# Optimization experiments

Measured on AMD Instinct MI355X. Metric: run time of the kernel, lower is better.

The kernel has to match this reference:

```python
import jax, jax.numpy as jnp
import numpy as np

N_NODES = 100000
N_EDGES = 800000
IN_DIM = 128
HID_DIM = 128


def setup_inputs() -> dict:
    key = jax.random.key(0)
    ks = jax.random.split(key, 10)
    s = 0.05
    return {
        "x": jax.random.normal(ks[0], (N_NODES, IN_DIM), dtype=jnp.float32),
        "edge_index": jax.random.randint(ks[1], (2, N_EDGES), 0, N_NODES, dtype=jnp.int64),
        "W1l": jax.random.normal(ks[2], (HID_DIM, IN_DIM), dtype=jnp.float32) * s,
        "b1": jax.random.normal(ks[3], (HID_DIM,), dtype=jnp.float32) * s,
        "W1r": jax.random.normal(ks[4], (HID_DIM, IN_DIM), dtype=jnp.float32) * s,
        "W2l": jax.random.normal(ks[5], (HID_DIM, HID_DIM), dtype=jnp.float32) * s,
        "b2": jax.random.normal(ks[6], (HID_DIM,), dtype=jnp.float32) * s,
        "W2r": jax.random.normal(ks[7], (HID_DIM, HID_DIM), dtype=jnp.float32) * s,
        "Wfc": jax.random.normal(ks[8], (1, HID_DIM), dtype=jnp.float32) * s,
        "bfc": jax.random.normal(ks[9], (1,), dtype=jnp.float32) * s,
    }


def _sage_conv(h, src, dst, n_nodes, Wl, b, Wr):
    # PyG SAGEConv (mean aggr): lin_l(mean_{j in N(i)} x_j) + lin_r(x_i)
    msg = h[src]  # [E, D] gather from source nodes
    agg = jax.ops.segment_sum(msg, dst, num_segments=n_nodes)  # [N, D]
    cnt = jax.ops.segment_sum(jnp.ones((src.shape[0], 1), h.dtype), dst,
                              num_segments=n_nodes)  # [N, 1]
    mean = agg / jnp.maximum(cnt, 1.0)  # isolated nodes -> 0 (matches scatter-mean)
    return mean @ Wl.T + b + h @ Wr.T


def reference(x, edge_index, W1l, b1, W1r, W2l, b2, W2r, Wfc, bfc):
    src, dst = edge_index[0], edge_index[1]
    n = x.shape[0]
    h = jax.nn.relu(_sage_conv(x, src, dst, n, W1l, b1, W1r))
    h = jax.nn.relu(_sage_conv(h, src, dst, n, W2l, b2, W2r))
    # dropout is identity in eval mode
    out = h @ Wfc.T + bfc  # [N, 1]
    return out.squeeze(-1)  # [N]
```

## Files before the change

### kernel.cpp

```cpp
#include <hip/hip_runtime.h>

#define N_NODES 100000
#define N_EDGES 800000
#define DIM 128

#define NB 391
#define BKCAP 2560
#define EPB 2048
#define BINB ((N_EDGES + EPB - 1) / EPB)
#define NXD (N_NODES * DIM / 2)

typedef __attribute__((ext_vector_type(8))) short short8;
typedef __attribute__((ext_vector_type(4))) float float4v;
typedef __attribute__((ext_vector_type(2))) float float2v;
typedef __attribute__((ext_vector_type(4))) unsigned int uint4v;

__device__ __forceinline__ float lo16(unsigned int v) {
    return __uint_as_float(v << 16);
}
__device__ __forceinline__ float hi16(unsigned int v) {
    return __uint_as_float(v & 0xffff0000u);
}
__device__ __forceinline__ float2v unp(unsigned int v) {
    return (float2v){lo16(v), hi16(v)};
}
__device__ __forceinline__ unsigned short f2bf(float f) {
    unsigned int x = __float_as_uint(f);
    unsigned int r = x + 0x7fffu + ((x >> 16) & 1u);
    return (unsigned short)(r >> 16);
}
__device__ __forceinline__ unsigned int packbf(float a, float b) {
    return (unsigned int)f2bf(a) | ((unsigned int)f2bf(b) << 16);
}

__device__ __forceinline__ int wave_iscan(int x, int lane) {
#pragma unroll
    for (int off = 1; off < 64; off <<= 1) {
        int n = __shfl_up(x, off, 64);
        x += (lane >= off) ? n : 0;
    }
    return x;
}


__global__ void edet_kernel(const int* __restrict__ edge, int* __restrict__ flags,
                            int* __restrict__ cur) {
    int i = blockIdx.x * blockDim.x + threadIdx.x;
    if (i < NB) cur[i] = 0;
    if (edge[2 * i + 1] != 0) flags[1] = 1;
}


__device__ __forceinline__ void load_edge(const int* __restrict__ edge, int eflag, int e,
                                          int& s, int& d) {
    if (eflag == 0) {
        s = edge[2 * e];
        d = edge[2 * (N_EDGES + e)];
    } else {
        s = edge[e];
        d = edge[N_EDGES + e];
    }
}


__global__ __launch_bounds__(256) void binconv_kernel(
    const int* __restrict__ edge, const int* __restrict__ flags, int* __restrict__ cur,
    unsigned int* __restrict__ pairs, const float* __restrict__ x,
    const float* __restrict__ wa, const float* __restrict__ wb,
    const float* __restrict__ wc, const float* __restrict__ wd,
    unsigned int* __restrict__ xdst, unsigned int* __restrict__ wdst) {
    int t = threadIdx.x;
    if (blockIdx.x >= BINB) {
        int i = (blockIdx.x - BINB) * 256 + t;
        if (i < NXD) {
            float2 v = ((const float2*)x)[i];
            xdst[i] = packbf(v.x, v.y);
        } else {
            int j = i - NXD;
            if (j < 4 * 8192) {
                int m = j >> 13, r = j & 8191;
                const float* src = (m == 0) ? wa : (m == 1) ? wb : (m == 2) ? wc : wd;
                float2 v = ((const float2*)src)[r];
                wdst[j] = packbf(v.x, v.y);
            }
        }
        return;
    }
    __shared__ int lcnt[NB];
    __shared__ int lbase[NB];
    for (int i = t; i < NB; i += 256) lcnt[i] = 0;
    __syncthreads();
    int e0 = blockIdx.x * EPB;
    int eflag = (flags[1] == 1) ? 1 : 0;
    int vb[8];
    unsigned int vp[8];
    bool valid[8];
#pragma unroll
    for (int k = 0; k < 8; ++k) {
        int e = e0 + k * 256 + t;
        valid[k] = false;
        if (e < N_EDGES) {
            int s, d;
            load_edge(edge, eflag, e, s, d);
            if ((unsigned)s < N_NODES && (unsigned)d < N_NODES) {
                valid[k] = true;
                vb[k] = d >> 8;
                vp[k] = ((unsigned int)s << 8) | (unsigned int)(d & 255);
                atomicAdd(&lcnt[vb[k]], 1);
            }
        }
    }
    __syncthreads();
    for (int i = t; i < NB; i += 256) {
        int c = lcnt[i];
        lbase[i] = (c > 0) ? atomicAdd(&cur[i], c) : 0;
        lcnt[i] = 0;
    }
    __syncthreads();
#pragma unroll
    for (int k = 0; k < 8; ++k) {
        if (valid[k]) {
            int b = vb[k];
            int pos = lbase[b] + atomicAdd(&lcnt[b], 1);
            if (pos < BKCAP)
                pairs[(size_t)b * BKCAP + pos] = vp[k];
        }
    }
}


__global__ __launch_bounds__(256) void csr_kernel(const int* __restrict__ cur,
                                                  const unsigned int* __restrict__ pairs,
                                                  int* __restrict__ rowptr,
                                                  int* __restrict__ esrc) {
    __shared__ int sh[512];
    __shared__ int hist[256];
    __shared__ int wsum[8];
    int b = blockIdx.x, t = threadIdx.x;
    int lane = t & 63, wv = t >> 6;
    int e0 = 2 * t, e1 = 2 * t + 1;
    int v0 = (e0 < NB) ? min(cur[e0], BKCAP) : 0;
    int v1 = (e1 < NB) ? min(cur[e1], BKCAP) : 0;
    int p = wave_iscan(v0 + v1, lane);
    if (lane == 63) wsum[wv] = p;
    hist[t] = 0;
    __syncthreads();
    int wpre = 0;
#pragma unroll
    for (int w = 0; w < 4; ++w) wpre += (w < wv) ? wsum[w] : 0;
    int incl1 = wpre + p;
    sh[e0] = incl1 - v1;
    sh[e1] = incl1;
    __syncthreads();
    int n = min(cur[b], BKCAP);
    int base = sh[b] - n;
    if (b == 0 && t == 0) rowptr[N_NODES] = sh[NB - 1];
    const unsigned int* pp = pairs + (size_t)b * BKCAP;
    for (int i = t; i < n; i += 256) atomicAdd(&hist[pp[i] & 255u], 1);
    __syncthreads();
    int v = hist[t];
    int ix = wave_iscan(v, lane);
    if (lane == 63) wsum[4 + wv] = ix;
    __syncthreads();
    int wpre2 = 0;
#pragma unroll
    for (int w = 0; w < 4; ++w) wpre2 += (w < wv) ? wsum[4 + w] : 0;
    int excl = wpre2 + ix - v;
    int node = b * 256 + t;
    if (node < N_NODES) rowptr[node] = base + excl;
    hist[t] = excl;
    __syncthreads();
    for (int i = t; i < n; i += 256) {
        unsigned int pk = pp[i];
        int pos = atomicAdd(&hist[pk & 255u], 1);
        esrc[base + pos] = (int)(pk >> 8);
    }
}


__global__ __launch_bounds__(256) void agg_kernel(const unsigned int* __restrict__ feat2,
                                                  const int* __restrict__ rowptr,
                                                  const int* __restrict__ esrc,
                                                  unsigned int* __restrict__ meanout) {
    int wid = (blockIdx.x * blockDim.x + threadIdx.x) >> 6;
    int lane = threadIdx.x & 63;
    int rowgrp = lane >> 4;
    int dimgrp = lane & 15;
    const int nwaves = 2048 * 4;
    for (int node = wid; node < N_NODES; node += nwaves) {
        int beg = rowptr[node], end = rowptr[node + 1];
        float2v a0 = {0.f, 0.f}, a1 = {0.f, 0.f}, a2 = {0.f, 0.f}, a3 = {0.f, 0.f};
        int e = beg;
        for (; e + 8 <= end; e += 8) {
            int s0 = esrc[e + rowgrp];
            int s1 = esrc[e + 4 + rowgrp];
            uint4v v0 = *(const uint4v*)(feat2 + (size_t)s0 * 64 + dimgrp * 4);
            uint4v v1 = *(const uint4v*)(feat2 + (size_t)s1 * 64 + dimgrp * 4);
            a0 += unp(v0.x) + unp(v1.x);
            a1 += unp(v0.y) + unp(v1.y);
            a2 += unp(v0.z) + unp(v1.z);
            a3 += unp(v0.w) + unp(v1.w);
        }
        if (e < end) {
            int i0 = e + rowgrp, i1 = e + 4 + rowgrp;
            bool ok0 = i0 < end, ok1 = i1 < end;
            int s0 = esrc[ok0 ? i0 : end - 1];
            int s1 = esrc[ok1 ? i1 : end - 1];
            uint4v v0 = *(const uint4v*)(feat2 + (size_t)s0 * 64 + dimgrp * 4);
            uint4v v1 = *(const uint4v*)(feat2 + (size_t)s1 * 64 + dimgrp * 4);
            float m0 = ok0 ? 1.f : 0.f, m1 = ok1 ? 1.f : 0.f;
            float2v m0v = {m0, m0}, m1v = {m1, m1};
            a0 += m0v * unp(v0.x) + m1v * unp(v1.x);
            a1 += m0v * unp(v0.y) + m1v * unp(v1.y);
            a2 += m0v * unp(v0.z) + m1v * unp(v1.z);
            a3 += m0v * unp(v0.w) + m1v * unp(v1.w);
        }
        float2v s0v = (rowgrp & 1) ? a0 : a1;
        float2v k0v = (rowgrp & 1) ? a1 : a0;
        float2v s2v = (rowgrp & 1) ? a2 : a3;
        float2v k2v = (rowgrp & 1) ? a3 : a2;
        k0v.x += __shfl_xor(s0v.x, 16, 64);
        k0v.y += __shfl_xor(s0v.y, 16, 64);
        k2v.x += __shfl_xor(s2v.x, 16, 64);
        k2v.y += __shfl_xor(s2v.y, 16, 64);
        float2v sv = (rowgrp & 2) ? k0v : k2v;
        float2v kv = (rowgrp & 2) ? k2v : k0v;
        kv.x += __shfl_xor(sv.x, 32, 64);
        kv.y += __shfl_xor(sv.y, 32, 64);
        int deg = end - beg;
        float sc = deg > 0 ? 1.f / (float)deg : 0.f;
        meanout[(size_t)node * 64 + dimgrp * 4 + rowgrp] = packbf(kv.x * sc, kv.y * sc);
    }
}


template <int FUSE_FC>
__global__ __launch_bounds__(256, 2) void gemm_kernel(
    const unsigned short* __restrict__ A0, const unsigned short* __restrict__ A1,
    const unsigned int* __restrict__ Wpk,
    const float* __restrict__ bias, const float* __restrict__ wfc,
    const float* __restrict__ bfc, unsigned short* __restrict__ hout,
    float* __restrict__ out) {
    __shared__ unsigned int wlds[16384];

    {
        int mat = threadIdx.x >> 7, row = threadIdx.x & 127;
        const unsigned int* g = Wpk + mat * 8192 + row * 64;
        unsigned int* lbase = wlds + mat * 8192;
#pragma unroll
        for (int q = 0; q < 16; ++q) {
            uint4v v = *(const uint4v*)(g + q * 4);
            *(uint4v*)(lbase + ((q * 128 + row) << 2)) = v;
        }
    }
    __syncthreads();

    int wave = threadIdx.x >> 6;
    int lane = threadIdx.x & 63;
    int lrow = lane & 15;
    int qsel = lane >> 4;
    int rowBase = blockIdx.x * 256 + wave * 64;

    float4v acc[4][8];
#pragma unroll
    for (int mt = 0; mt < 4; ++mt)
#pragma unroll
        for (int nt = 0; nt < 8; ++nt) acc[mt][nt] = (float4v){0.f, 0.f, 0.f, 0.f};

    const unsigned short* Ah[2] = {A0, A1};
    int r4a[4];
#pragma unroll
    for (int mt = 0; mt < 4; ++mt) {
        int r = rowBase + mt * 16 + lrow;
        r4a[mt] = (r >= N_NODES) ? (N_NODES - 1) : r;
    }

    short8 a[3][4];
#pragma unroll
    for (int mt = 0; mt < 4; ++mt) {
        a[0][mt] = *(const short8*)(A0 + (size_t)r4a[mt] * DIM + qsel * 8);
        a[1][mt] = *(const short8*)(A0 + (size_t)r4a[mt] * DIM + 32 + qsel * 8);
        a[2][mt] = *(const short8*)(A0 + (size_t)r4a[mt] * DIM + 64 + qsel * 8);
    }

#pragma unroll
    for (int step = 0; step < 8; ++step) {
        int half = step >> 2, kt = step & 3;
        int slot = step % 3;
        short8 cur[4];
#pragma unroll
        for (int mt = 0; mt < 4; ++mt) cur[mt] = a[slot][mt];
        if (step < 5) {
            int ns = step + 3;
            int nk0 = (ns & 3) * 32 + qsel * 8;
            const unsigned short* A = Ah[ns >> 2];
#pragma unroll
            for (int mt = 0; mt < 4; ++mt)
                a[slot][mt] = *(const short8*)(A + (size_t)r4a[mt] * DIM + nk0);
        }
        const unsigned int* lbase = wlds + half * 8192;
        int qg = kt * 4 + qsel;
#pragma unroll
        for (int nt = 0; nt < 8; ++nt) {
            short8 b = *(const short8*)(lbase + ((qg * 128 + nt * 16 + lrow) << 2));
#pragma unroll
            for (int mt = 0; mt < 4; ++mt)
                acc[mt][nt] = __builtin_amdgcn_mfma_f32_16x16x32_bf16(cur[mt], b, acc[mt][nt], 0, 0, 0);
        }
    }

    int crow0 = (lane >> 4) * 4;
    if (!FUSE_FC) {
#pragma unroll
        for (int mt = 0; mt < 4; ++mt) {
#pragma unroll
            for (int nt = 0; nt < 8; ++nt) {
                int col = nt * 16 + lrow;
                float bv = bias[col];
#pragma unroll
                for (int r4 = 0; r4 < 4; ++r4) {
                    int row = rowBase + mt * 16 + crow0 + r4;
                    if (row < N_NODES) {
                        float v = acc[mt][nt][r4] + bv;
                        hout[(size_t)row * DIM + col] = f2bf(v > 0.f ? v : 0.f);
                    }
                }
            }
        }
    } else {
        float bv[8], wv[8];
#pragma unroll
        for (int nt = 0; nt < 8; ++nt) {
            bv[nt] = bias[nt * 16 + lrow];
            wv[nt] = wfc[nt * 16 + lrow];
        }
        float bf0 = bfc[0];
#pragma unroll
        for (int mt = 0; mt < 4; ++mt) {
#pragma unroll
            for (int r4 = 0; r4 < 4; ++r4) {
                float p = 0.f;
#pragma unroll
                for (int nt = 0; nt < 8; ++nt) {
                    float v = acc[mt][nt][r4] + bv[nt];
                    p += (v > 0.f ? v : 0.f) * wv[nt];
                }
#pragma unroll
                for (int off = 1; off < 16; off <<= 1) p += __shfl_xor(p, off, 64);
                int row = rowBase + mt * 16 + crow0 + r4;
                if (lrow == 0 && row < N_NODES) out[row] = p + bf0;
            }
        }
    }
}


extern "C" void kernel_launch(void* const* d_in, const int* in_sizes, int n_in,
                              void* d_out, int out_size, void* d_ws, size_t ws_size,
                              hipStream_t stream) {
    const float* x  = (const float*)d_in[0];
    const int* edge = (const int*)d_in[1];
    const float* W1l = (const float*)d_in[2];
    const float* b1  = (const float*)d_in[3];
    const float* W1r = (const float*)d_in[4];
    const float* W2l = (const float*)d_in[5];
    const float* b2  = (const float*)d_in[6];
    const float* W2r = (const float*)d_in[7];
    const float* Wfc = (const float*)d_in[8];
    const float* bfc = (const float*)d_in[9];
    float* out = (float*)d_out;

    char* ws = (char*)d_ws;
    size_t off = 0;
    int* flags  = (int*)(ws + off); off += 256;
    int* rowptr = (int*)(ws + off); off += ((size_t)N_NODES + 64) * 4;
    int* esrc   = (int*)(ws + off); off += (size_t)N_EDGES * 4;
    int* cur    = (int*)(ws + off); off += (size_t)NB * 4 + 256;
    off = (off + 255) & ~(size_t)255;
    unsigned int* pairs = (unsigned int*)(ws + off); off += (size_t)NB * BKCAP * 4;
    off = (off + 255) & ~(size_t)255;
    unsigned int* wbf = (unsigned int*)(ws + off); off += 4 * 8192 * 4;
    off = (off + 255) & ~(size_t)255;
    unsigned short* xbf  = (unsigned short*)(ws + off); off += (size_t)N_NODES * DIM * 2;
    unsigned short* mean = (unsigned short*)(ws + off); off += (size_t)N_NODES * DIM * 2;
    unsigned short* h1   = (unsigned short*)(ws + off); off += (size_t)N_NODES * DIM * 2;

    const int gemmBlocks = (N_NODES + 255) / 256;
    const int convBlocks = (NXD + 4 * 8192 + 255) / 256;

    edet_kernel<<<16, 256, 0, stream>>>(edge, flags, cur);
    binconv_kernel<<<BINB + convBlocks, 256, 0, stream>>>(edge, flags, cur, pairs, x,
                                                          W1l, W1r, W2l, W2r,
                                                          (unsigned int*)xbf, wbf);
    csr_kernel<<<NB, 256, 0, stream>>>(cur, pairs, rowptr, esrc);

    agg_kernel<<<2048, 256, 0, stream>>>((const unsigned int*)xbf, rowptr, esrc,
                                         (unsigned int*)mean);
    gemm_kernel<0><<<gemmBlocks, 256, 0, stream>>>(mean, xbf, wbf, b1, nullptr, nullptr,
                                                   h1, nullptr);
    agg_kernel<<<2048, 256, 0, stream>>>((const unsigned int*)h1, rowptr, esrc,
                                         (unsigned int*)mean);
    gemm_kernel<1><<<gemmBlocks, 256, 0, stream>>>(mean, h1, wbf + 2 * 8192, b2, Wfc, bfc,
                                                   nullptr, out);
}
```

Before: 239.6 us.

## Drop edge-detect kernel, vectorize bf16 conversion, prefetch next row pointers

Removes the separate edge-format detection kernel. Each binning block now detects int64-vs-int32 layout locally with a wave vote, and the bucket counter is cleared with a memset. The fp32-to-bf16 conversion of x and the weights now reads float4 and writes two packed words per thread, halving the thread count. The aggregation loop prefetches the next node's rowptr bounds before processing the current node, hiding that load latency. The per-block format check only looks at the first 256 edges of its own chunk, which is a heuristic that could disagree across blocks.

```diff
diff --git a/kernel.cpp b/kernel.cpp
--- a/kernel.cpp
+++ b/kernel.cpp
@@ -8,12 +8,14 @@
 #define BKCAP 2560
 #define EPB 2048
 #define BINB ((N_EDGES + EPB - 1) / EPB)
-#define NXD (N_NODES * DIM / 2)
+#define NXF (N_NODES * DIM / 4)
+#define WF4 (4 * 4096)
 
 typedef __attribute__((ext_vector_type(8))) short short8;
 typedef __attribute__((ext_vector_type(4))) float float4v;
 typedef __attribute__((ext_vector_type(2))) float float2v;
 typedef __attribute__((ext_vector_type(4))) unsigned int uint4v;
+typedef __attribute__((ext_vector_type(2))) unsigned int uint2v;
 
 __device__ __forceinline__ float lo16(unsigned int v) {
     return __uint_as_float(v << 16);
@@ -40,14 +42,6 @@
         x += (lane >= off) ? n : 0;
     }
     return x;
-}
-
-
-__global__ void edet_kernel(const int* __restrict__ edge, int* __restrict__ flags,
-                            int* __restrict__ cur) {
-    int i = blockIdx.x * blockDim.x + threadIdx.x;
-    if (i < NB) cur[i] = 0;
-    if (edge[2 * i + 1] != 0) flags[1] = 1;
 }
 
 
@@ -64,7 +58,7 @@
 
 
 __global__ __launch_bounds__(256) void binconv_kernel(
-    const int* __restrict__ edge, const int* __restrict__ flags, int* __restrict__ cur,
+    const int* __restrict__ edge, int* __restrict__ cur,
     unsigned int* __restrict__ pairs, const float* __restrict__ x,
     const float* __restrict__ wa, const float* __restrict__ wb,
     const float* __restrict__ wc, const float* __restrict__ wd,
@@ -72,16 +66,18 @@
     int t = threadIdx.x;
     if (blockIdx.x >= BINB) {
         int i = (blockIdx.x - BINB) * 256 + t;
-        if (i < NXD) {
-            float2 v = ((const float2*)x)[i];
-            xdst[i] = packbf(v.x, v.y);
+        if (i < NXF) {
+            float4 v = ((const float4*)x)[i];
+            uint2v o = {packbf(v.x, v.y), packbf(v.z, v.w)};
+            *(uint2v*)(xdst + 2 * (size_t)i) = o;
         } else {
-            int j = i - NXD;
-            if (j < 4 * 8192) {
-                int m = j >> 13, r = j & 8191;
+            int j = i - NXF;
+            if (j < WF4) {
+                int m = j >> 12, r = j & 4095;
                 const float* src = (m == 0) ? wa : (m == 1) ? wb : (m == 2) ? wc : wd;
-                float2 v = ((const float2*)src)[r];
-                wdst[j] = packbf(v.x, v.y);
+                float4 v = ((const float4*)src)[r];
+                uint2v o = {packbf(v.x, v.y), packbf(v.z, v.w)};
+                *(uint2v*)(wdst + (size_t)m * 8192 + 2 * r) = o;
             }
         }
         return;
@@ -89,9 +85,9 @@
     __shared__ int lcnt[NB];
     __shared__ int lbase[NB];
     for (int i = t; i < NB; i += 256) lcnt[i] = 0;
-    __syncthreads();
     int e0 = blockIdx.x * EPB;
-    int eflag = (flags[1] == 1) ? 1 : 0;
+    int eflag = __any(edge[2 * (e0 + t) + 1] != 0) ? 1 : 0;
+    __syncthreads();
     int vb[8];
     unsigned int vp[8];
     bool valid[8];
@@ -187,8 +183,15 @@
     int rowgrp = lane >> 4;
     int dimgrp = lane & 15;
     const int nwaves = 2048 * 4;
-    for (int node = wid; node < N_NODES; node += nwaves) {
-        int beg = rowptr[node], end = rowptr[node + 1];
+    int node = wid;
+    int beg = rowptr[node], end = rowptr[node + 1];
+    while (1) {
+        int nn = node + nwaves;
+        int nbg = 0, nen = 0;
+        if (nn < N_NODES) {
+            nbg = rowptr[nn];
+            nen = rowptr[nn + 1];
+        }
         float2v a0 = {0.f, 0.f}, a1 = {0.f, 0.f}, a2 = {0.f, 0.f}, a3 = {0.f, 0.f};
         int e = beg;
         for (; e + 8 <= end; e += 8) {
@@ -230,6 +233,10 @@
         int deg = end - beg;
         float sc = deg > 0 ? 1.f / (float)deg : 0.f;
         meanout[(size_t)node * 64 + dimgrp * 4 + rowgrp] = packbf(kv.x * sc, kv.y * sc);
+        if (nn >= N_NODES) break;
+        node = nn;
+        beg = nbg;
+        end = nen;
     }
 }
 
@@ -372,7 +379,6 @@
 
     char* ws = (char*)d_ws;
     size_t off = 0;
-    int* flags  = (int*)(ws + off); off += 256;
     int* rowptr = (int*)(ws + off); off += ((size_t)N_NODES + 64) * 4;
     int* esrc   = (int*)(ws + off); off += (size_t)N_EDGES * 4;
     int* cur    = (int*)(ws + off); off += (size_t)NB * 4 + 256;
@@ -386,10 +392,10 @@
     unsigned short* h1   = (unsigned short*)(ws + off); off += (size_t)N_NODES * DIM * 2;
 
     const int gemmBlocks = (N_NODES + 255) / 256;
-    const int convBlocks = (NXD + 4 * 8192 + 255) / 256;
-
-    edet_kernel<<<16, 256, 0, stream>>>(edge, flags, cur);
-    binconv_kernel<<<BINB + convBlocks, 256, 0, stream>>>(edge, flags, cur, pairs, x,
+    const int convBlocks = (NXF + WF4 + 255) / 256;
+
+    hipMemsetAsync(cur, 0, NB * sizeof(int), stream);
+    binconv_kernel<<<BINB + convBlocks, 256, 0, stream>>>(edge, cur, pairs, x,
                                                           W1l, W1r, W2l, W2r,
                                                           (unsigned int*)xbf, wbf);
     csr_kernel<<<NB, 256, 0, stream>>>(cur, pairs, rowptr, esrc);
```

After: 239.7 us. No clear change (+0.1%).
